# Performance work log

Hardware: AMD Instinct MI355X
Metric: run time of the kernel (lower is better)

The kernel has to match this reference:

```python
import jax, jax.numpy as jnp
import numpy as np

L, B, T, C, H, V, CTX = 4, 2, 1024, 1024, 16, 50257, 2048
D = C // H
EPS = 1e-5
NEG_SLOPE = 0.01


def layer_norm(x, w, b):
    mu = jnp.mean(x, axis=-1, keepdims=True)
    var = jnp.mean(jnp.square(x - mu), axis=-1, keepdims=True)
    return (x - mu) * jax.lax.rsqrt(var + EPS) * w + b


def setup_inputs() -> dict:
    key = jax.random.key(0)
    ks = jax.random.split(key, 8)
    s = 0.02  # init std as in _init_weights
    return {
        "idx": jax.random.randint(ks[0], (B, T), 0, V),
        "wte": jax.random.normal(ks[1], (V, C), jnp.float32) * s,
        "wpe": jax.random.normal(ks[2], (CTX, C), jnp.float32) * s,
        "ln1_w": jnp.ones((L, C), jnp.float32),
        "ln1_b": jnp.zeros((L, C), jnp.float32),
        "attn_w": jax.random.normal(ks[3], (L, C, 3 * C), jnp.float32) * s,
        "attn_b": jnp.zeros((L, 3 * C), jnp.float32),
        "proj_w": jax.random.normal(ks[4], (L, C, C), jnp.float32) * s,
        "proj_b": jnp.zeros((L, C), jnp.float32),
        "ln2_w": jnp.ones((L, C), jnp.float32),
        "ln2_b": jnp.zeros((L, C), jnp.float32),
        "fc_w": jax.random.normal(ks[5], (L, C, 4 * C), jnp.float32) * s,
        "fc_b": jnp.zeros((L, 4 * C), jnp.float32),
        "fcproj_w": jax.random.normal(ks[6], (L, 4 * C, C), jnp.float32) * s,
        "fcproj_b": jnp.zeros((L, C), jnp.float32),
        "lnf_w": jnp.ones((C,), jnp.float32),
        "lnf_b": jnp.zeros((C,), jnp.float32),
    }


def reference(idx, wte, wpe, ln1_w, ln1_b, attn_w, attn_b, proj_w, proj_b,
              ln2_w, ln2_b, fc_w, fc_b, fcproj_w, fcproj_b, lnf_w, lnf_b):
    t = idx.shape[1]
    x = wte[idx] + wpe[:t]  # [B,T,C]; dropout=0 => identity
    causal = jnp.tril(jnp.ones((t, t), bool))  # [T,T]
    scale = 1.0 / np.sqrt(D)
    for l in range(L):
        # --- causal self-attention ---
        h = layer_norm(x, ln1_w[l], ln1_b[l])
        qkv = h @ attn_w[l] + attn_b[l]  # [B,T,3C]
        q, k, v = jnp.split(qkv, 3, axis=-1)
        q = q.reshape(B, t, H, D)
        k = k.reshape(B, t, H, D)
        v = v.reshape(B, t, H, D)
        att = jnp.einsum('bthd,bshd->bhts', q, k) * scale  # [B,H,T,T]
        att = jnp.where(causal, att, -jnp.inf)
        att = jax.nn.softmax(att, axis=-1)
        y = jnp.einsum('bhts,bshd->bthd', att, v).reshape(B, t, C)
        x = x + y @ proj_w[l] + proj_b[l]
        # --- MLP ---
        h = layer_norm(x, ln2_w[l], ln2_b[l])
        h = h @ fc_w[l] + fc_b[l]
        h = jnp.where(h >= 0, h, NEG_SLOPE * h)  # LeakyReLU(0.01)
        x = x + h @ fcproj_w[l] + fcproj_b[l]
    x = layer_norm(x, lnf_w, lnf_b)
    # targets=None path: lm_head on last position only, tied weight = wte
    logits = x[:, -1:, :] @ wte.T  # [B,1,V]
    return logits
```

## Files before the change

kernel.cpp:

```cpp
#include <hip/hip_runtime.h>
#include <hip/hip_bf16.h>


#define TT 1024
#define CC 1024
#define NHEAD 16
#define DHEAD 64
#define NBATCH 2
#define VOCAB 50257

typedef __attribute__((ext_vector_type(8))) short bf16x8;
typedef __attribute__((ext_vector_type(4))) float f32x4;
typedef __attribute__((ext_vector_type(16))) float f32x16;

#define GPTR(p) (const __attribute__((address_space(1))) void*)(p)
#define LPTR(p) (__attribute__((address_space(3))) void*)(p)

__device__ __forceinline__ unsigned short f2bf(float f) {
  union { float f; unsigned u; } v; v.f = f;
  unsigned r = v.u + 0x7fffu + ((v.u >> 16) & 1u);
  return (unsigned short)(r >> 16);
}
__device__ __forceinline__ float bf2f(unsigned short u) {
  union { unsigned u; float f; } v; v.u = ((unsigned)u) << 16;
  return v.f;
}

__device__ __forceinline__ f32x4 mfma_bf16(bf16x8 a, bf16x8 b, f32x4 c) {
  return __builtin_amdgcn_mfma_f32_16x16x32_bf16(a, b, c, 0, 0, 0);
}
__device__ __forceinline__ f32x16 mfma32_bf16(bf16x8 a, bf16x8 b, f32x16 c) {
  return __builtin_amdgcn_mfma_f32_32x32x16_bf16(a, b, c, 0, 0, 0);
}

__device__ __forceinline__ unsigned pk2(float lo, float hi) {
  return (unsigned)f2bf(lo) | ((unsigned)f2bf(hi) << 16);
}

__global__ __launch_bounds__(256) void embedln_k(const int* __restrict__ idx,
    const float* __restrict__ wte, const float* __restrict__ wpe,
    const float* __restrict__ lw, const float* __restrict__ lb,
    float* __restrict__ x, unsigned short* __restrict__ h)
{
  __shared__ float rs[4], rss[4];
  const int row = blockIdx.x;
  const int t = row & (TT - 1);
  const int tok = idx[row];
  const int tid = threadIdx.x, wave = tid >> 6, lane = tid & 63;
  float4 va = ((const float4*)(wte + (size_t)tok * CC))[tid];
  float4 vp = ((const float4*)(wpe + (size_t)t * CC))[tid];
  float4 v = make_float4(va.x + vp.x, va.y + vp.y, va.z + vp.z, va.w + vp.w);
  ((float4*)(x + (size_t)row * CC))[tid] = v;
  float s  = v.x + v.y + v.z + v.w;
  float ss = v.x*v.x + v.y*v.y + v.z*v.z + v.w*v.w;
#pragma unroll
  for (int off = 1; off < 64; off <<= 1) {
    s  += __shfl_xor(s, off, 64);
    ss += __shfl_xor(ss, off, 64);
  }
  if (lane == 0) { rs[wave] = s; rss[wave] = ss; }
  __syncthreads();
  s  = rs[0] + rs[1] + rs[2] + rs[3];
  ss = rss[0] + rss[1] + rss[2] + rss[3];
  float mu = s * (1.f / CC);
  float var = ss * (1.f / CC) - mu * mu;
  float rstd = rsqrtf(var + 1e-5f);
  float4 wv = ((const float4*)lw)[tid];
  float4 bv = ((const float4*)lb)[tid];
  float o0 = (v.x - mu) * rstd * wv.x + bv.x;
  float o1 = (v.y - mu) * rstd * wv.y + bv.y;
  float o2 = (v.z - mu) * rstd * wv.z + bv.z;
  float o3 = (v.w - mu) * rstd * wv.w + bv.w;
  ((uint2*)(h + (size_t)row * CC))[tid] = make_uint2(pk2(o0, o1), pk2(o2, o3));
}

__global__ __launch_bounds__(256) void redln_k(float* __restrict__ x,
    const unsigned short* __restrict__ P, const float* __restrict__ bias,
    const float* __restrict__ lw, const float* __restrict__ lb,
    unsigned short* __restrict__ out, int splits)
{
  int row = blockIdx.x * 4 + (threadIdx.x >> 6);
  int lane = threadIdx.x & 63;
  const int c0 = lane * 16;
  float* xw = x + (size_t)row * CC + c0;
  float4 v[4];
#pragma unroll
  for (int i = 0; i < 4; ++i) v[i] = *(const float4*)(xw + i * 4);
  {
    const float4* b4 = (const float4*)(bias + c0);
#pragma unroll
    for (int i = 0; i < 4; ++i) {
      float4 bv = b4[i];
      v[i].x += bv.x; v[i].y += bv.y; v[i].z += bv.z; v[i].w += bv.w;
    }
  }
  for (int sp = 0; sp < splits; ++sp) {
    const unsigned short* pp = P + ((size_t)sp * 2048 + row) * CC + c0;
    bf16x8 pa = *(const bf16x8*)pp;
    bf16x8 pb = *(const bf16x8*)(pp + 8);
    v[0].x += bf2f((unsigned short)pa[0]); v[0].y += bf2f((unsigned short)pa[1]);
    v[0].z += bf2f((unsigned short)pa[2]); v[0].w += bf2f((unsigned short)pa[3]);
    v[1].x += bf2f((unsigned short)pa[4]); v[1].y += bf2f((unsigned short)pa[5]);
    v[1].z += bf2f((unsigned short)pa[6]); v[1].w += bf2f((unsigned short)pa[7]);
    v[2].x += bf2f((unsigned short)pb[0]); v[2].y += bf2f((unsigned short)pb[1]);
    v[2].z += bf2f((unsigned short)pb[2]); v[2].w += bf2f((unsigned short)pb[3]);
    v[3].x += bf2f((unsigned short)pb[4]); v[3].y += bf2f((unsigned short)pb[5]);
    v[3].z += bf2f((unsigned short)pb[6]); v[3].w += bf2f((unsigned short)pb[7]);
  }
  float s = 0.f, ss = 0.f;
#pragma unroll
  for (int i = 0; i < 4; ++i) {
    *(float4*)(xw + i * 4) = v[i];
    s  += v[i].x + v[i].y + v[i].z + v[i].w;
    ss += v[i].x*v[i].x + v[i].y*v[i].y + v[i].z*v[i].z + v[i].w*v[i].w;
  }
#pragma unroll
  for (int off = 1; off < 64; off <<= 1) {
    s  += __shfl_xor(s, off, 64);
    ss += __shfl_xor(ss, off, 64);
  }
  float mu = s * (1.f / CC);
  float var = ss * (1.f / CC) - mu * mu;
  float rstd = rsqrtf(var + 1e-5f);
  const float* wr = lw + c0;
  const float* br = lb + c0;
  unsigned q[8];
#pragma unroll
  for (int i = 0; i < 4; ++i) {
    float4 wv = *(const float4*)(wr + i * 4);
    float4 bv = *(const float4*)(br + i * 4);
    float o0 = (v[i].x - mu) * rstd * wv.x + bv.x;
    float o1 = (v[i].y - mu) * rstd * wv.y + bv.y;
    float o2 = (v[i].z - mu) * rstd * wv.z + bv.z;
    float o3 = (v[i].w - mu) * rstd * wv.w + bv.w;
    q[i*2+0] = pk2(o0, o1);
    q[i*2+1] = pk2(o2, o3);
  }
  uint4* op = (uint4*)(out + (size_t)row * CC + c0);
  op[0] = make_uint4(q[0], q[1], q[2], q[3]);
  op[1] = make_uint4(q[4], q[5], q[6], q[7]);
}

__global__ __launch_bounds__(256) void wconv_all_k(
    const float* __restrict__ attn_w, unsigned short* __restrict__ wt_attn,
    const float* __restrict__ proj_w, unsigned short* __restrict__ wt_proj,
    const float* __restrict__ fc_w,   unsigned short* __restrict__ wt_fc,
    const float* __restrict__ fcp_w,  unsigned short* __restrict__ wt_fcp)
{
  int b = blockIdx.x;
  const float* W; unsigned short* Wt; int K, N, kx, ny;
  if (b < 3072) {
    int layer = b / 768, tI = b % 768;
    K = 1024; N = 3072;
    W = attn_w + (size_t)layer * K * N; Wt = wt_attn + (size_t)layer * K * N;
    kx = tI % 16; ny = tI / 16;
  } else if (b < 3840) {
    b -= 3072; int layer = b / 256, tI = b % 256;
    K = 1024; N = 1024;
    W = proj_w + (size_t)layer * K * N; Wt = wt_proj + (size_t)layer * K * N;
    kx = tI % 16; ny = tI / 16;
  } else if (b < 6912) {
    b -= 3840; int layer = b / 1024, tI = b % 1024;
    K = 1024; N = 4096;
    W = fc_w + (size_t)layer * K * N; Wt = wt_fc + (size_t)layer * K * N;
    kx = tI % 16; ny = tI / 16;
  } else {
    b -= 6912; int layer = b / 1024, tI = b % 1024;
    K = 4096; N = 1024;
    W = fcp_w + (size_t)layer * K * N; Wt = wt_fcp + (size_t)layer * K * N;
    kx = tI % 64; ny = tI / 64;
  }
  __shared__ float tile[64][65];
  const int k0 = kx << 6, n0 = ny << 6;
  const int t = threadIdx.x;
  {
    const int r = t >> 4, c4 = t & 15;
#pragma unroll
    for (int p = 0; p < 4; ++p) {
      int kr = r + (p << 4);
      float4 v = *(const float4*)(W + (size_t)(k0 + kr) * N + n0 + (c4 << 2));
      tile[kr][(c4 << 2) + 0] = v.x;
      tile[kr][(c4 << 2) + 1] = v.y;
      tile[kr][(c4 << 2) + 2] = v.z;
      tile[kr][(c4 << 2) + 3] = v.w;
    }
  }
  __syncthreads();
  {
    const int n = t >> 2, kq = t & 3;
    bf16x8 o0, o1;
#pragma unroll
    for (int e = 0; e < 8; ++e) o0[e] = (short)f2bf(tile[(kq << 4) + e][n]);
#pragma unroll
    for (int e = 0; e < 8; ++e) o1[e] = (short)f2bf(tile[(kq << 4) + 8 + e][n]);
    unsigned short* dst = Wt + (size_t)(n0 + n) * K + k0 + (kq << 4);
    *(bf16x8*)dst = o0;
    *(bf16x8*)(dst + 8) = o1;
  }
}

#define MODE_QKV  0
#define MODE_PART 1
#define MODE_FC   2

template<int MODE>
__global__ __launch_bounds__(256, 4) void gemm_k(
    const unsigned short* __restrict__ A,
    const unsigned short* __restrict__ Wt,
    const float* __restrict__ bias,
    unsigned short* __restrict__ obf,
    unsigned short* __restrict__ q_o,
    unsigned short* __restrict__ k_o,
    unsigned short* __restrict__ v_o,
    int M, int N, int K, int kchunk, int ncol0)
{
  __shared__ alignas(16) unsigned short Asm[128 * 64];
  __shared__ alignas(16) unsigned short Bsm[128 * 64];
  const int tid  = threadIdx.x;
  const int wave = tid >> 6, lane = tid & 63;
  const int rl = lane & 31, hi = lane >> 5;
  const int nTM = M >> 7, nTN = N >> 7;
  int bid = blockIdx.x;
  const int mt = bid % nTM; bid /= nTM;
  const int nt = bid % nTN;
  const int s  = bid / nTN;
  const int m0 = mt << 7, n0 = nt << 7;
  const int kb = s * kchunk;
  const int nIter = kchunk >> 6;
  const int wm = (wave >> 1) << 6, wn = (wave & 1) << 6;
  f32x16 acc[2][2] = {};

#define STAGE(K0)                                                             \
  {                                                                           \
    _Pragma("unroll")                                                         \
    for (int c = 0; c < 4; ++c) {                                             \
      const int seg = (wave << 2) + c;                                        \
      const int g = (seg << 6) + lane;                                        \
      const int row = g >> 3, kq = g & 7;                                     \
      const int kqs = kq ^ (row & 7);                                         \
      const unsigned short* asrc = A  + (size_t)(m0 + row) * K + (K0) + (kqs << 3); \
      const unsigned short* bsrc = Wt + (size_t)(n0 + row) * K + (K0) + (kqs << 3); \
      __builtin_amdgcn_global_load_lds(GPTR(asrc), LPTR(&Asm[seg << 9]), 16, 0, 0); \
      __builtin_amdgcn_global_load_lds(GPTR(bsrc), LPTR(&Bsm[seg << 9]), 16, 0, 0); \
    }                                                                         \
  }

  for (int t = 0; t < nIter; ++t) {
    STAGE(kb + (t << 6));
    __syncthreads();
#pragma unroll
    for (int sl = 0; sl < 4; ++sl) {
      const int c = sl * 2 + hi;
      const int cs = (c ^ (rl & 7)) << 3;
      bf16x8 a0 = *(const bf16x8*)(Asm + ((wm + rl) << 6) + cs);
      bf16x8 a1 = *(const bf16x8*)(Asm + ((wm + 32 + rl) << 6) + cs);
      bf16x8 b0 = *(const bf16x8*)(Bsm + ((wn + rl) << 6) + cs);
      bf16x8 b1 = *(const bf16x8*)(Bsm + ((wn + 32 + rl) << 6) + cs);
      acc[0][0] = mfma32_bf16(a0, b0, acc[0][0]);
      acc[0][1] = mfma32_bf16(a0, b1, acc[0][1]);
      acc[1][0] = mfma32_bf16(a1, b0, acc[1][0]);
      acc[1][1] = mfma32_bf16(a1, b1, acc[1][1]);
    }
    __syncthreads();
  }
#undef STAGE

#pragma unroll
  for (int j = 0; j < 2; ++j) {
    int gc = n0 + wn + j * 32 + rl;
    int gcol = ncol0 + gc;
    float bv = (MODE == MODE_PART) ? 0.f : bias[gcol];
#pragma unroll
    for (int i = 0; i < 2; ++i) {
      int gr0 = m0 + wm + i * 32 + 4 * hi;
#pragma unroll
      for (int reg = 0; reg < 16; ++reg) {
        int grow = gr0 + (reg & 3) + 8 * (reg >> 2);
        float val = acc[i][j][reg] + bv;
        if (MODE == MODE_QKV) {
          int which = gcol >> 10;
          int head = (gcol >> 6) & 15;
          int d = gcol & 63;
          int bb = grow >> 10, tt2 = grow & (TT - 1);
          size_t bhb = ((size_t)((bb << 4) + head)) << 16;
          if (which == 2)      v_o[bhb + ((size_t)d << 10) + tt2] = f2bf(val);
          else if (which == 1) k_o[bhb + ((size_t)tt2 << 6) + d] = f2bf(val);
          else                 q_o[bhb + ((size_t)tt2 << 6) + d] = f2bf(val);
        } else if (MODE == MODE_FC) {
          val = (val >= 0.f) ? val : 0.01f * val;
          obf[(size_t)grow * N + gc] = f2bf(val);
        } else {
          obf[((size_t)s * M + grow) * N + gc] = f2bf(val);
        }
      }
    }
  }
}

__global__ __launch_bounds__(256) void attn_k(
    const unsigned short* __restrict__ Qb,
    const unsigned short* __restrict__ Kb,
    const unsigned short* __restrict__ Vb,
    unsigned short* __restrict__ ybuf)
{
  __shared__ alignas(16) unsigned short Ksm[64][72];
  __shared__ alignas(16) unsigned short Vtsm[64][64];
  __shared__ alignas(16) unsigned short Psm[4][16][72];
  const int tid = threadIdx.x;
  const int wave = tid >> 6, lane = tid & 63;
  const int lg = lane >> 4, ll = lane & 15;
  const int qt = blockIdx.x & 15, bh = blockIdx.x >> 4;
  const int b = bh >> 4, h = bh & 15;
  const size_t base = (size_t)bh << 16;
  const int q0 = qt << 6;
  const float SC = 0.125f * 1.44269504f;

  const int qrow = q0 + wave * 16 + ll;
  bf16x8 aq0 = *(const bf16x8*)(Qb + base + ((size_t)qrow << 6) + (lg << 3));
  bf16x8 aq1 = *(const bf16x8*)(Qb + base + ((size_t)qrow << 6) + 32 + (lg << 3));

  f32x4 accy[4] = {};
  float m_run[4], l_run[4];
#pragma unroll
  for (int r = 0; r < 4; ++r) { m_run[r] = -1e30f; l_run[r] = 0.f; }

  const int sk_row = tid >> 3, sk_cq = tid & 7;
  const int sv_d = tid & 63, sv_kq = tid >> 6;
  const int qg0 = q0 + wave * 16 + (lg << 2);

  for (int kb = 0; kb <= qt; ++kb) {
    const int kbase = kb << 6;
#pragma unroll
    for (int p = 0; p < 2; ++p) {
      int r = sk_row + (p << 5);
      bf16x8 kv = *(const bf16x8*)(Kb + base + ((size_t)(kbase + r) << 6) + (sk_cq << 3));
      *(bf16x8*)&Ksm[r][sk_cq << 3] = kv;
    }
#pragma unroll
    for (int p = 0; p < 2; ++p) {
      int kq8 = sv_kq + (p << 2);
      bf16x8 wv = *(const bf16x8*)(Vb + base + ((size_t)sv_d << 10) + kbase + (kq8 << 3));
      int u = kq8 ^ (sv_d & 7);
      *(bf16x8*)&Vtsm[sv_d][u << 3] = wv;
    }
    __syncthreads();

    float p_[4][4];
    float rmax[4] = {-1e30f, -1e30f, -1e30f, -1e30f};
    __builtin_amdgcn_s_setprio(1);
#pragma unroll
    for (int kk = 0; kk < 4; ++kk) {
      f32x4 z = {};
      bf16x8 bk0 = *(const bf16x8*)&Ksm[kk * 16 + ll][lg << 3];
      bf16x8 bk1 = *(const bf16x8*)&Ksm[kk * 16 + ll][32 + (lg << 3)];
      z = mfma_bf16(aq0, bk0, z);
      z = mfma_bf16(aq1, bk1, z);
      int key = kbase + kk * 16 + ll;
#pragma unroll
      for (int r = 0; r < 4; ++r) {
        float v = z[r] * SC;
        v = (key > qg0 + r) ? -1e30f : v;
        p_[kk][r] = v;
        rmax[r] = fmaxf(rmax[r], v);
      }
    }
    __builtin_amdgcn_s_setprio(0);
#pragma unroll
    for (int off = 1; off < 16; off <<= 1)
#pragma unroll
      for (int r = 0; r < 4; ++r)
        rmax[r] = fmaxf(rmax[r], __shfl_xor(rmax[r], off, 64));

    float alpha[4], rsum[4];
#pragma unroll
    for (int r = 0; r < 4; ++r) {
      float mn = fmaxf(m_run[r], rmax[r]);
      alpha[r] = exp2f(m_run[r] - mn);
      m_run[r] = mn;
      rsum[r] = 0.f;
    }
#pragma unroll
    for (int kk = 0; kk < 4; ++kk)
#pragma unroll
      for (int r = 0; r < 4; ++r) {
        float e = exp2f(p_[kk][r] - m_run[r]);
        p_[kk][r] = e;
        rsum[r] += e;
      }
#pragma unroll
    for (int off = 1; off < 16; off <<= 1)
#pragma unroll
      for (int r = 0; r < 4; ++r)
        rsum[r] += __shfl_xor(rsum[r], off, 64);
#pragma unroll
    for (int r = 0; r < 4; ++r)
      l_run[r] = l_run[r] * alpha[r] + rsum[r];
#pragma unroll
    for (int df = 0; df < 4; ++df)
#pragma unroll
      for (int r = 0; r < 4; ++r)
        accy[df][r] *= alpha[r];

#pragma unroll
    for (int kk = 0; kk < 4; ++kk)
#pragma unroll
      for (int r = 0; r < 4; ++r)
        Psm[wave][(lg << 2) + r][kk * 16 + ll] = f2bf(p_[kk][r]);
    bf16x8 pa0 = *(const bf16x8*)&Psm[wave][ll][lg << 3];
    bf16x8 pa1 = *(const bf16x8*)&Psm[wave][ll][32 + (lg << 3)];

    __builtin_amdgcn_s_setprio(1);
#pragma unroll
    for (int df = 0; df < 4; ++df) {
      int d = df * 16 + ll;
      int u0 = lg ^ (d & 7);
      int u1 = (4 + lg) ^ (d & 7);
      bf16x8 bv0 = *(const bf16x8*)&Vtsm[d][u0 << 3];
      bf16x8 bv1 = *(const bf16x8*)&Vtsm[d][u1 << 3];
      accy[df] = mfma_bf16(pa0, bv0, accy[df]);
      accy[df] = mfma_bf16(pa1, bv1, accy[df]);
    }
    __builtin_amdgcn_s_setprio(0);
    __syncthreads();
  }

#pragma unroll
  for (int df = 0; df < 4; ++df)
#pragma unroll
    for (int r = 0; r < 4; ++r) {
      int qr = qg0 + r;
      float y = accy[df][r] / l_run[r];
      ybuf[(((size_t)((b << 10) + qr)) << 10) + (h << 6) + df * 16 + ll] = f2bf(y);
    }
}


__global__ __launch_bounds__(256) void qlast_k(
    const unsigned short* __restrict__ hbuf,
    const float* __restrict__ Wq,
    float* __restrict__ qpart)
{
  __shared__ float xs[2][128];
  const int tid = threadIdx.x, ks = blockIdx.y;
  {
    const int b = tid >> 7, j = tid & 127;
    xs[b][j] = bf2f(hbuf[((size_t)(b * TT + TT - 1)) * CC + ks * 128 + j]);
  }
  __syncthreads();
  const int n = blockIdx.x * 256 + tid;
  float a0 = 0.f, a1 = 0.f;
  const float* wp = Wq + (size_t)(ks * 128) * 3072 + n;
  for (int k = 0; k < 128; k += 8)
#pragma unroll
    for (int u = 0; u < 8; ++u) {
      float w = wp[(size_t)(k + u) * 3072];
      a0 += xs[0][k + u] * w;
      a1 += xs[1][k + u] * w;
    }
  qpart[(size_t)(ks * 2 + 0) * 1024 + n] = a0;
  qpart[(size_t)(ks * 2 + 1) * 1024 + n] = a1;
}

__global__ __launch_bounds__(256) void attnlast2_k(
    const float* __restrict__ qpart, const float* __restrict__ bq,
    const unsigned short* __restrict__ Kb,
    const unsigned short* __restrict__ Vb,
    float* __restrict__ y_last)
{
  __shared__ float qs[64];
  __shared__ float wm[4], wl[4], wacc[4][64];
  const int tid = threadIdx.x;
  const int wave = tid >> 6, lane = tid & 63;
  const int bh = blockIdx.x;
  const int b = bh >> 4, h = bh & 15;
  const size_t base = (size_t)bh << 16;
  if (tid < 64) {
    const int col = h * 64 + tid;
    float q = bq[col];
#pragma unroll
    for (int ks = 0; ks < 8; ++ks)
      q += qpart[(size_t)(ks * 2 + b) * 1024 + col];
    qs[tid] = q;
  }
  __syncthreads();

  float m_w = -1e30f, l_w = 0.f, acc = 0.f;
  for (int ks = 0; ks < 4; ++ks) {
    const int key = ks * 256 + wave * 64 + lane;
    float s = 0.f;
    const unsigned short* kp = Kb + base + ((size_t)key << 6);
#pragma unroll
    for (int o = 0; o < 8; ++o) {
      bf16x8 kv = *(const bf16x8*)(kp + (o << 3));
#pragma unroll
      for (int e = 0; e < 8; ++e)
        s += qs[(o << 3) + e] * bf2f((unsigned short)kv[e]);
    }
    s *= 0.125f;
    float m = s;
#pragma unroll
    for (int off = 1; off < 64; off <<= 1)
      m = fmaxf(m, __shfl_xor(m, off, 64));
    float mn = fmaxf(m_w, m);
    float alpha = __expf(m_w - mn);
    m_w = mn;
    float p = __expf(s - mn);
    float ps = p;
#pragma unroll
    for (int off = 1; off < 64; off <<= 1)
      ps += __shfl_xor(ps, off, 64);
    l_w = l_w * alpha + ps;
    float a2 = 0.f;
    const unsigned short* vp = Vb + base + ((size_t)lane << 10) + ks * 256 + wave * 64;
#pragma unroll
    for (int j8 = 0; j8 < 8; ++j8) {
      bf16x8 vv = *(const bf16x8*)(vp + (j8 << 3));
#pragma unroll
      for (int e = 0; e < 8; ++e) {
        float pj = __shfl(p, (j8 << 3) + e, 64);
        a2 += pj * bf2f((unsigned short)vv[e]);
      }
    }
    acc = acc * alpha + a2;
  }
  if (lane == 0) { wm[wave] = m_w; wl[wave] = l_w; }
  wacc[wave][lane] = acc;
  __syncthreads();
  if (wave == 0) {
    float m0 = fmaxf(fmaxf(wm[0], wm[1]), fmaxf(wm[2], wm[3]));
    float lt = 0.f, at = 0.f;
#pragma unroll
    for (int sI = 0; sI < 4; ++sI) {
      float f = __expf(wm[sI] - m0);
      lt += wl[sI] * f;
      at += wacc[sI][lane] * f;
    }
    y_last[b * CC + h * 64 + lane] = at / lt;
  }
}

__global__ __launch_bounds__(256) void projpart_k(
    const float* __restrict__ ylast,
    const float* __restrict__ W,
    float* __restrict__ ppart)
{
  __shared__ float xs[2][128];
  const int tid = threadIdx.x, ks = blockIdx.y;
  {
    const int b = tid >> 7, j = tid & 127;
    xs[b][j] = ylast[b * 1024 + ks * 128 + j];
  }
  __syncthreads();
  const int n = blockIdx.x * 256 + tid;
  float a0 = 0.f, a1 = 0.f;
  const float* wp = W + (size_t)(ks * 128) * 1024 + n;
  for (int k = 0; k < 128; k += 8)
#pragma unroll
    for (int u = 0; u < 8; ++u) {
      float w = wp[(size_t)(k + u) * 1024];
      a0 += xs[0][k + u] * w;
      a1 += xs[1][k + u] * w;
    }
  ppart[(size_t)(ks * 2 + 0) * 1024 + n] = a0;
  ppart[(size_t)(ks * 2 + 1) * 1024 + n] = a1;
}

__global__ __launch_bounds__(256) void fclast_k(
    const float* __restrict__ x, const float* __restrict__ ppart,
    const float* __restrict__ pbias,
    const float* __restrict__ lw, const float* __restrict__ lb,
    const float* __restrict__ W,
    float* __restrict__ fcpart)
{
  __shared__ float xs[2][1024];
  const int tid = threadIdx.x;
  const int wave = tid >> 6, lane = tid & 63;
  if (wave < 2) {
    const int c0 = lane * 16;
    const float* xr = x + ((size_t)(wave * TT + TT - 1)) * CC + c0;
    float4 v[4];
    float s = 0.f, ss = 0.f;
#pragma unroll
    for (int i = 0; i < 4; ++i) {
      v[i] = *(const float4*)(xr + i * 4);
      float4 bv = *(const float4*)(pbias + c0 + i * 4);
      v[i].x += bv.x; v[i].y += bv.y; v[i].z += bv.z; v[i].w += bv.w;
    }
#pragma unroll
    for (int sp = 0; sp < 8; ++sp) {
      const float* pp = ppart + (size_t)(sp * 2 + wave) * 1024 + c0;
#pragma unroll
      for (int i = 0; i < 4; ++i) {
        float4 pv = *(const float4*)(pp + i * 4);
        v[i].x += pv.x; v[i].y += pv.y; v[i].z += pv.z; v[i].w += pv.w;
      }
    }
#pragma unroll
    for (int i = 0; i < 4; ++i) {
      s  += v[i].x + v[i].y + v[i].z + v[i].w;
      ss += v[i].x*v[i].x + v[i].y*v[i].y + v[i].z*v[i].z + v[i].w*v[i].w;
    }
#pragma unroll
    for (int off = 1; off < 64; off <<= 1) {
      s  += __shfl_xor(s, off, 64);
      ss += __shfl_xor(ss, off, 64);
    }
    float mu = s * (1.f / CC);
    float var = ss * (1.f / CC) - mu * mu;
    float rstd = rsqrtf(var + 1e-5f);
#pragma unroll
    for (int i = 0; i < 4; ++i) {
      float4 wv = *(const float4*)(lw + c0 + i * 4);
      float4 bv = *(const float4*)(lb + c0 + i * 4);
      xs[wave][c0 + i * 4 + 0] = (v[i].x - mu) * rstd * wv.x + bv.x;
      xs[wave][c0 + i * 4 + 1] = (v[i].y - mu) * rstd * wv.y + bv.y;
      xs[wave][c0 + i * 4 + 2] = (v[i].z - mu) * rstd * wv.z + bv.z;
      xs[wave][c0 + i * 4 + 3] = (v[i].w - mu) * rstd * wv.w + bv.w;
    }
  }
  __syncthreads();
  const int ks = blockIdx.y;
  const int n = blockIdx.x * 256 + tid;
  float a0 = 0.f, a1 = 0.f;
  const float* wp = W + (size_t)(ks * 128) * 4096 + n;
  for (int k = 0; k < 128; k += 8)
#pragma unroll
    for (int u = 0; u < 8; ++u) {
      float w = wp[(size_t)(k + u) * 4096];
      a0 += xs[0][ks * 128 + k + u] * w;
      a1 += xs[1][ks * 128 + k + u] * w;
    }
  fcpart[(size_t)(ks * 2 + 0) * 4096 + n] = a0;
  fcpart[(size_t)(ks * 2 + 1) * 4096 + n] = a1;
}

__global__ __launch_bounds__(256) void fcprojpart_k(
    const float* __restrict__ fcpart, const float* __restrict__ fcbias,
    const float* __restrict__ W,
    float* __restrict__ fppart)
{
  __shared__ float hs[2][512];
  const int tid = threadIdx.x, ks = blockIdx.y;
#pragma unroll
  for (int i = 0; i < 4; ++i) {
    const int e = tid + 256 * i;
    const int b = e >> 9, j = e & 511;
    const int c = ks * 512 + j;
    float v = fcbias[c];
#pragma unroll
    for (int sp = 0; sp < 8; ++sp)
      v += fcpart[(size_t)(sp * 2 + b) * 4096 + c];
    hs[b][j] = (v >= 0.f) ? v : 0.01f * v;
  }
  __syncthreads();
  const int n = blockIdx.x * 256 + tid;
  float a0 = 0.f, a1 = 0.f;
  const float* wp = W + (size_t)(ks * 512) * 1024 + n;
  for (int k = 0; k < 512; k += 8)
#pragma unroll
    for (int u = 0; u < 8; ++u) {
      float w = wp[(size_t)(k + u) * 1024];
      a0 += hs[0][k + u] * w;
      a1 += hs[1][k + u] * w;
    }
  fppart[(size_t)(ks * 2 + 0) * 1024 + n] = a0;
  fppart[(size_t)(ks * 2 + 1) * 1024 + n] = a1;
}

__global__ __launch_bounds__(256) void lnfmerge_k(const float* __restrict__ x,
    const float* __restrict__ ppart, const float* __restrict__ pbias,
    const float* __restrict__ fppart, const float* __restrict__ fpbias,
    const float* __restrict__ lw, const float* __restrict__ lb,
    float* __restrict__ xf)
{
  __shared__ float rs[4], rss[4];
  const int row = blockIdx.x;
  const int tid = threadIdx.x;
  const int wave = tid >> 6, lane = tid & 63;
  const int c0 = tid * 4;
  float4 v = *(const float4*)(x + ((size_t)(row * TT + TT - 1)) * CC + c0);
  {
    float4 b1 = *(const float4*)(pbias + c0);
    float4 b2 = *(const float4*)(fpbias + c0);
    v.x += b1.x + b2.x; v.y += b1.y + b2.y;
    v.z += b1.z + b2.z; v.w += b1.w + b2.w;
  }
#pragma unroll
  for (int sp = 0; sp < 8; ++sp) {
    float4 a = *(const float4*)(ppart + (size_t)(sp * 2 + row) * 1024 + c0);
    float4 b = *(const float4*)(fppart + (size_t)(sp * 2 + row) * 1024 + c0);
    v.x += a.x + b.x; v.y += a.y + b.y;
    v.z += a.z + b.z; v.w += a.w + b.w;
  }
  float s  = v.x + v.y + v.z + v.w;
  float ss = v.x*v.x + v.y*v.y + v.z*v.z + v.w*v.w;
#pragma unroll
  for (int off = 1; off < 64; off <<= 1) {
    s  += __shfl_xor(s, off, 64);
    ss += __shfl_xor(ss, off, 64);
  }
  if (lane == 0) { rs[wave] = s; rss[wave] = ss; }
  __syncthreads();
  s  = rs[0] + rs[1] + rs[2] + rs[3];
  ss = rss[0] + rss[1] + rss[2] + rss[3];
  float mu = s * (1.f / CC);
  float var = ss * (1.f / CC) - mu * mu;
  float rstd = rsqrtf(var + 1e-5f);
  float4 wv = *(const float4*)(lw + c0);
  float4 bv = *(const float4*)(lb + c0);
  float4 o;
  o.x = (v.x - mu) * rstd * wv.x + bv.x;
  o.y = (v.y - mu) * rstd * wv.y + bv.y;
  o.z = (v.z - mu) * rstd * wv.z + bv.z;
  o.w = (v.w - mu) * rstd * wv.w + bv.w;
  *(float4*)(xf + (size_t)row * CC + c0) = o;
}

__global__ __launch_bounds__(256) void head_k(const float* __restrict__ xf,
    const float* __restrict__ wte, float* __restrict__ out)
{
  int v = (blockIdx.x << 2) + (threadIdx.x >> 6);
  if (v >= VOCAB) return;
  int lane = threadIdx.x & 63;
  const float4* wr = (const float4*)(wte + (size_t)v * CC);
  const float4* x0 = (const float4*)xf;
  const float4* x1 = (const float4*)(xf + CC);
  float a0 = 0.f, a1 = 0.f;
#pragma unroll
  for (int i = 0; i < 4; ++i) {
    float4 wv = wr[lane + i * 64];
    float4 p0 = x0[lane + i * 64];
    float4 p1 = x1[lane + i * 64];
    a0 += wv.x * p0.x + wv.y * p0.y + wv.z * p0.z + wv.w * p0.w;
    a1 += wv.x * p1.x + wv.y * p1.y + wv.z * p1.z + wv.w * p1.w;
  }
#pragma unroll
  for (int off = 1; off < 64; off <<= 1) {
    a0 += __shfl_xor(a0, off, 64);
    a1 += __shfl_xor(a1, off, 64);
  }
  if (lane == 0) {
    out[v] = a0;
    out[VOCAB + v] = a1;
  }
}

extern "C" void kernel_launch(void* const* d_in, const int* in_sizes, int n_in,
                              void* d_out, int out_size, void* d_ws, size_t ws_size,
                              hipStream_t stream)
{
  const int*   idx      = (const int*)d_in[0];
  const float* wte      = (const float*)d_in[1];
  const float* wpe      = (const float*)d_in[2];
  const float* ln1_w    = (const float*)d_in[3];
  const float* ln1_b    = (const float*)d_in[4];
  const float* attn_w   = (const float*)d_in[5];
  const float* attn_b   = (const float*)d_in[6];
  const float* proj_w   = (const float*)d_in[7];
  const float* proj_b   = (const float*)d_in[8];
  const float* ln2_w    = (const float*)d_in[9];
  const float* ln2_b    = (const float*)d_in[10];
  const float* fc_w     = (const float*)d_in[11];
  const float* fc_b     = (const float*)d_in[12];
  const float* fcproj_w = (const float*)d_in[13];
  const float* fcproj_b = (const float*)d_in[14];
  const float* lnf_w    = (const float*)d_in[15];
  const float* lnf_b    = (const float*)d_in[16];
  float* out = (float*)d_out;

  const size_t MB = 1u << 20;
  char* ws = (char*)d_ws;
  float*          x   = (float*)ws;
  unsigned short* h   = (unsigned short*)(ws + 8*MB);
  unsigned short* qb  = (unsigned short*)(ws + 12*MB);
  unsigned short* kb_ = (unsigned short*)(ws + 16*MB);
  unsigned short* vb  = (unsigned short*)(ws + 20*MB);
  unsigned short* yb  = (unsigned short*)(ws + 24*MB);
  unsigned short* hf  = (unsigned short*)(ws + 28*MB);
  char* sm = ws + 44*MB;
  float* xf     = (float*)(sm + 0);
  float* ylast  = (float*)(sm + 16*1024);
  float* qpart  = (float*)(sm + 64*1024);
  float* ppart  = (float*)(sm + 128*1024);
  float* fppart = (float*)(sm + 192*1024);
  float* fcpart = (float*)(sm + 256*1024);
  unsigned short* wt_attn   = (unsigned short*)(ws + 46*MB);
  unsigned short* wt_proj   = (unsigned short*)(ws + 70*MB);
  unsigned short* wt_fc     = (unsigned short*)(ws + 76*MB);
  unsigned short* wt_fcproj = (unsigned short*)(ws + 100*MB);
  unsigned short* Ppart     = (unsigned short*)(ws + 124*MB);

  embedln_k<<<NBATCH * TT, 256, 0, stream>>>(idx, wte, wpe, ln1_w, ln1_b, x, h);

  wconv_all_k<<<9984, 256, 0, stream>>>(attn_w, wt_attn, proj_w, wt_proj,
                                        fc_w, wt_fc, fcproj_w, wt_fcproj);

  for (int l = 0; l < 3; ++l) {
    gemm_k<MODE_QKV><<<16 * 24, 256, 0, stream>>>(h,
        wt_attn + (size_t)l * 3072 * 1024, attn_b + (size_t)l * 3 * CC,
        nullptr, qb, kb_, vb, 2048, 3072, 1024, 1024, 0);
    attn_k<<<NBATCH * NHEAD * 16, 256, 0, stream>>>(qb, kb_, vb, yb);
    gemm_k<MODE_PART><<<16 * 8 * 4, 256, 0, stream>>>(yb,
        wt_proj + (size_t)l * 1024 * 1024, nullptr,
        Ppart, nullptr, nullptr, nullptr, 2048, 1024, 1024, 256, 0);
    redln_k<<<512, 256, 0, stream>>>(x, Ppart, proj_b + l * CC,
        ln2_w + l * CC, ln2_b + l * CC, h, 4);
    gemm_k<MODE_FC><<<16 * 32, 256, 0, stream>>>(h,
        wt_fc + (size_t)l * 1024 * 4096, fc_b + (size_t)l * 4 * CC,
        hf, nullptr, nullptr, nullptr, 2048, 4096, 1024, 1024, 0);
    gemm_k<MODE_PART><<<16 * 8 * 4, 256, 0, stream>>>(hf,
        wt_fcproj + (size_t)l * 4096 * 1024, nullptr,
        Ppart, nullptr, nullptr, nullptr, 2048, 1024, 4096, 1024, 0);
    redln_k<<<512, 256, 0, stream>>>(x, Ppart, fcproj_b + l * CC,
        ln1_w + (l + 1) * CC, ln1_b + (l + 1) * CC, h, 4);
  }

  {
    const int l = 3;
    gemm_k<MODE_QKV><<<16 * 16, 256, 0, stream>>>(h,
        wt_attn + (size_t)l * 3072 * 1024 + (size_t)1024 * 1024,
        attn_b + (size_t)l * 3 * CC,
        nullptr, qb, kb_, vb, 2048, 2048, 1024, 1024, 1024);
    qlast_k<<<dim3(4, 8), 256, 0, stream>>>(h,
        attn_w + (size_t)l * CC * 3 * CC, qpart);
    attnlast2_k<<<32, 256, 0, stream>>>(qpart, attn_b + (size_t)l * 3 * CC,
        kb_, vb, ylast);
    projpart_k<<<dim3(4, 8), 256, 0, stream>>>(ylast,
        proj_w + (size_t)l * CC * CC, ppart);
    fclast_k<<<dim3(16, 8), 256, 0, stream>>>(x, ppart, proj_b + l * CC,
        ln2_w + l * CC, ln2_b + l * CC,
        fc_w + (size_t)l * CC * 4 * CC, fcpart);
    fcprojpart_k<<<dim3(4, 8), 256, 0, stream>>>(fcpart,
        fc_b + (size_t)l * 4 * CC, fcproj_w + (size_t)l * 4 * CC * CC, fppart);
    lnfmerge_k<<<2, 256, 0, stream>>>(x, ppart, proj_b + l * CC,
        fppart, fcproj_b + l * CC, lnf_w, lnf_b, xf);
  }

  head_k<<<(VOCAB + 3) / 4, 256, 0, stream>>>(xf, wte, out);
}
```

Measured before the change: 644.9 us.

## Fuse embed+weight-convert launches; widen attention key tile and skip rescale

```diff
diff --git a/kernel.cpp b/kernel.cpp
--- a/kernel.cpp
+++ b/kernel.cpp
@@ -37,117 +37,50 @@
   return (unsigned)f2bf(lo) | ((unsigned)f2bf(hi) << 16);
 }
 
-__global__ __launch_bounds__(256) void embedln_k(const int* __restrict__ idx,
+__global__ __launch_bounds__(256) void prep_k(const int* __restrict__ idx,
     const float* __restrict__ wte, const float* __restrict__ wpe,
     const float* __restrict__ lw, const float* __restrict__ lb,
-    float* __restrict__ x, unsigned short* __restrict__ h)
-{
-  __shared__ float rs[4], rss[4];
-  const int row = blockIdx.x;
-  const int t = row & (TT - 1);
-  const int tok = idx[row];
-  const int tid = threadIdx.x, wave = tid >> 6, lane = tid & 63;
-  float4 va = ((const float4*)(wte + (size_t)tok * CC))[tid];
-  float4 vp = ((const float4*)(wpe + (size_t)t * CC))[tid];
-  float4 v = make_float4(va.x + vp.x, va.y + vp.y, va.z + vp.z, va.w + vp.w);
-  ((float4*)(x + (size_t)row * CC))[tid] = v;
-  float s  = v.x + v.y + v.z + v.w;
-  float ss = v.x*v.x + v.y*v.y + v.z*v.z + v.w*v.w;
-#pragma unroll
-  for (int off = 1; off < 64; off <<= 1) {
-    s  += __shfl_xor(s, off, 64);
-    ss += __shfl_xor(ss, off, 64);
-  }
-  if (lane == 0) { rs[wave] = s; rss[wave] = ss; }
-  __syncthreads();
-  s  = rs[0] + rs[1] + rs[2] + rs[3];
-  ss = rss[0] + rss[1] + rss[2] + rss[3];
-  float mu = s * (1.f / CC);
-  float var = ss * (1.f / CC) - mu * mu;
-  float rstd = rsqrtf(var + 1e-5f);
-  float4 wv = ((const float4*)lw)[tid];
-  float4 bv = ((const float4*)lb)[tid];
-  float o0 = (v.x - mu) * rstd * wv.x + bv.x;
-  float o1 = (v.y - mu) * rstd * wv.y + bv.y;
-  float o2 = (v.z - mu) * rstd * wv.z + bv.z;
-  float o3 = (v.w - mu) * rstd * wv.w + bv.w;
-  ((uint2*)(h + (size_t)row * CC))[tid] = make_uint2(pk2(o0, o1), pk2(o2, o3));
-}
-
-__global__ __launch_bounds__(256) void redln_k(float* __restrict__ x,
-    const unsigned short* __restrict__ P, const float* __restrict__ bias,
-    const float* __restrict__ lw, const float* __restrict__ lb,
-    unsigned short* __restrict__ out, int splits)
-{
-  int row = blockIdx.x * 4 + (threadIdx.x >> 6);
-  int lane = threadIdx.x & 63;
-  const int c0 = lane * 16;
-  float* xw = x + (size_t)row * CC + c0;
-  float4 v[4];
-#pragma unroll
-  for (int i = 0; i < 4; ++i) v[i] = *(const float4*)(xw + i * 4);
-  {
-    const float4* b4 = (const float4*)(bias + c0);
-#pragma unroll
-    for (int i = 0; i < 4; ++i) {
-      float4 bv = b4[i];
-      v[i].x += bv.x; v[i].y += bv.y; v[i].z += bv.z; v[i].w += bv.w;
-    }
-  }
-  for (int sp = 0; sp < splits; ++sp) {
-    const unsigned short* pp = P + ((size_t)sp * 2048 + row) * CC + c0;
-    bf16x8 pa = *(const bf16x8*)pp;
-    bf16x8 pb = *(const bf16x8*)(pp + 8);
-    v[0].x += bf2f((unsigned short)pa[0]); v[0].y += bf2f((unsigned short)pa[1]);
-    v[0].z += bf2f((unsigned short)pa[2]); v[0].w += bf2f((unsigned short)pa[3]);
-    v[1].x += bf2f((unsigned short)pa[4]); v[1].y += bf2f((unsigned short)pa[5]);
-    v[1].z += bf2f((unsigned short)pa[6]); v[1].w += bf2f((unsigned short)pa[7]);
-    v[2].x += bf2f((unsigned short)pb[0]); v[2].y += bf2f((unsigned short)pb[1]);
-    v[2].z += bf2f((unsigned short)pb[2]); v[2].w += bf2f((unsigned short)pb[3]);
-    v[3].x += bf2f((unsigned short)pb[4]); v[3].y += bf2f((unsigned short)pb[5]);
-    v[3].z += bf2f((unsigned short)pb[6]); v[3].w += bf2f((unsigned short)pb[7]);
-  }
-  float s = 0.f, ss = 0.f;
-#pragma unroll
-  for (int i = 0; i < 4; ++i) {
-    *(float4*)(xw + i * 4) = v[i];
-    s  += v[i].x + v[i].y + v[i].z + v[i].w;
-    ss += v[i].x*v[i].x + v[i].y*v[i].y + v[i].z*v[i].z + v[i].w*v[i].w;
-  }
-#pragma unroll
-  for (int off = 1; off < 64; off <<= 1) {
-    s  += __shfl_xor(s, off, 64);
-    ss += __shfl_xor(ss, off, 64);
-  }
-  float mu = s * (1.f / CC);
-  float var = ss * (1.f / CC) - mu * mu;
-  float rstd = rsqrtf(var + 1e-5f);
-  const float* wr = lw + c0;
-  const float* br = lb + c0;
-  unsigned q[8];
-#pragma unroll
-  for (int i = 0; i < 4; ++i) {
-    float4 wv = *(const float4*)(wr + i * 4);
-    float4 bv = *(const float4*)(br + i * 4);
-    float o0 = (v[i].x - mu) * rstd * wv.x + bv.x;
-    float o1 = (v[i].y - mu) * rstd * wv.y + bv.y;
-    float o2 = (v[i].z - mu) * rstd * wv.z + bv.z;
-    float o3 = (v[i].w - mu) * rstd * wv.w + bv.w;
-    q[i*2+0] = pk2(o0, o1);
-    q[i*2+1] = pk2(o2, o3);
-  }
-  uint4* op = (uint4*)(out + (size_t)row * CC + c0);
-  op[0] = make_uint4(q[0], q[1], q[2], q[3]);
-  op[1] = make_uint4(q[4], q[5], q[6], q[7]);
-}
-
-__global__ __launch_bounds__(256) void wconv_all_k(
+    float* __restrict__ x, unsigned short* __restrict__ h,
     const float* __restrict__ attn_w, unsigned short* __restrict__ wt_attn,
     const float* __restrict__ proj_w, unsigned short* __restrict__ wt_proj,
     const float* __restrict__ fc_w,   unsigned short* __restrict__ wt_fc,
     const float* __restrict__ fcp_w,  unsigned short* __restrict__ wt_fcp)
 {
-  int b = blockIdx.x;
+  __shared__ float tile[64][65];
+  const int tid = threadIdx.x;
+  if (blockIdx.x < 2048) {
+    const int row = blockIdx.x;
+    const int t = row & (TT - 1);
+    const int tok = idx[row];
+    const int wave = tid >> 6, lane = tid & 63;
+    float4 va = ((const float4*)(wte + (size_t)tok * CC))[tid];
+    float4 vp = ((const float4*)(wpe + (size_t)t * CC))[tid];
+    float4 v = make_float4(va.x + vp.x, va.y + vp.y, va.z + vp.z, va.w + vp.w);
+    ((float4*)(x + (size_t)row * CC))[tid] = v;
+    float s  = v.x + v.y + v.z + v.w;
+    float ss = v.x*v.x + v.y*v.y + v.z*v.z + v.w*v.w;
+#pragma unroll
+    for (int off = 1; off < 64; off <<= 1) {
+      s  += __shfl_xor(s, off, 64);
+      ss += __shfl_xor(ss, off, 64);
+    }
+    if (lane == 0) { tile[0][wave] = s; tile[0][4 + wave] = ss; }
+    __syncthreads();
+    s  = tile[0][0] + tile[0][1] + tile[0][2] + tile[0][3];
+    ss = tile[0][4] + tile[0][5] + tile[0][6] + tile[0][7];
+    float mu = s * (1.f / CC);
+    float var = ss * (1.f / CC) - mu * mu;
+    float rstd = rsqrtf(var + 1e-5f);
+    float4 wv = ((const float4*)lw)[tid];
+    float4 bv = ((const float4*)lb)[tid];
+    float o0 = (v.x - mu) * rstd * wv.x + bv.x;
+    float o1 = (v.y - mu) * rstd * wv.y + bv.y;
+    float o2 = (v.z - mu) * rstd * wv.z + bv.z;
+    float o3 = (v.w - mu) * rstd * wv.w + bv.w;
+    ((uint2*)(h + (size_t)row * CC))[tid] = make_uint2(pk2(o0, o1), pk2(o2, o3));
+    return;
+  }
+  int b = blockIdx.x - 2048;
   const float* W; unsigned short* Wt; int K, N, kx, ny;
   if (b < 3072) {
     int layer = b / 768, tI = b % 768;
@@ -170,11 +103,9 @@
     W = fcp_w + (size_t)layer * K * N; Wt = wt_fcp + (size_t)layer * K * N;
     kx = tI % 64; ny = tI / 64;
   }
-  __shared__ float tile[64][65];
   const int k0 = kx << 6, n0 = ny << 6;
-  const int t = threadIdx.x;
   {
-    const int r = t >> 4, c4 = t & 15;
+    const int r = tid >> 4, c4 = tid & 15;
 #pragma unroll
     for (int p = 0; p < 4; ++p) {
       int kr = r + (p << 4);
@@ -187,7 +118,7 @@
   }
   __syncthreads();
   {
-    const int n = t >> 2, kq = t & 3;
+    const int n = tid >> 2, kq = tid & 3;
     bf16x8 o0, o1;
 #pragma unroll
     for (int e = 0; e < 8; ++e) o0[e] = (short)f2bf(tile[(kq << 4) + e][n]);
@@ -197,6 +128,73 @@
     *(bf16x8*)dst = o0;
     *(bf16x8*)(dst + 8) = o1;
   }
+}
+
+__global__ __launch_bounds__(256) void redln_k(float* __restrict__ x,
+    const unsigned short* __restrict__ P, const float* __restrict__ bias,
+    const float* __restrict__ lw, const float* __restrict__ lb,
+    unsigned short* __restrict__ out, int splits)
+{
+  int row = blockIdx.x * 4 + (threadIdx.x >> 6);
+  int lane = threadIdx.x & 63;
+  const int c0 = lane * 16;
+  float* xw = x + (size_t)row * CC + c0;
+  float4 v[4];
+#pragma unroll
+  for (int i = 0; i < 4; ++i) v[i] = *(const float4*)(xw + i * 4);
+  {
+    const float4* b4 = (const float4*)(bias + c0);
+#pragma unroll
+    for (int i = 0; i < 4; ++i) {
+      float4 bv = b4[i];
+      v[i].x += bv.x; v[i].y += bv.y; v[i].z += bv.z; v[i].w += bv.w;
+    }
+  }
+  for (int sp = 0; sp < splits; ++sp) {
+    const unsigned short* pp = P + ((size_t)sp * 2048 + row) * CC + c0;
+    bf16x8 pa = *(const bf16x8*)pp;
+    bf16x8 pb = *(const bf16x8*)(pp + 8);
+    v[0].x += bf2f((unsigned short)pa[0]); v[0].y += bf2f((unsigned short)pa[1]);
+    v[0].z += bf2f((unsigned short)pa[2]); v[0].w += bf2f((unsigned short)pa[3]);
+    v[1].x += bf2f((unsigned short)pa[4]); v[1].y += bf2f((unsigned short)pa[5]);
+    v[1].z += bf2f((unsigned short)pa[6]); v[1].w += bf2f((unsigned short)pa[7]);
+    v[2].x += bf2f((unsigned short)pb[0]); v[2].y += bf2f((unsigned short)pb[1]);
+    v[2].z += bf2f((unsigned short)pb[2]); v[2].w += bf2f((unsigned short)pb[3]);
+    v[3].x += bf2f((unsigned short)pb[4]); v[3].y += bf2f((unsigned short)pb[5]);
+    v[3].z += bf2f((unsigned short)pb[6]); v[3].w += bf2f((unsigned short)pb[7]);
+  }
+  float s = 0.f, ss = 0.f;
+#pragma unroll
+  for (int i = 0; i < 4; ++i) {
+    *(float4*)(xw + i * 4) = v[i];
+    s  += v[i].x + v[i].y + v[i].z + v[i].w;
+    ss += v[i].x*v[i].x + v[i].y*v[i].y + v[i].z*v[i].z + v[i].w*v[i].w;
+  }
+#pragma unroll
+  for (int off = 1; off < 64; off <<= 1) {
+    s  += __shfl_xor(s, off, 64);
+    ss += __shfl_xor(ss, off, 64);
+  }
+  float mu = s * (1.f / CC);
+  float var = ss * (1.f / CC) - mu * mu;
+  float rstd = rsqrtf(var + 1e-5f);
+  const float* wr = lw + c0;
+  const float* br = lb + c0;
+  unsigned q[8];
+#pragma unroll
+  for (int i = 0; i < 4; ++i) {
+    float4 wv = *(const float4*)(wr + i * 4);
+    float4 bv = *(const float4*)(br + i * 4);
+    float o0 = (v[i].x - mu) * rstd * wv.x + bv.x;
+    float o1 = (v[i].y - mu) * rstd * wv.y + bv.y;
+    float o2 = (v[i].z - mu) * rstd * wv.z + bv.z;
+    float o3 = (v[i].w - mu) * rstd * wv.w + bv.w;
+    q[i*2+0] = pk2(o0, o1);
+    q[i*2+1] = pk2(o2, o3);
+  }
+  uint4* op = (uint4*)(out + (size_t)row * CC + c0);
+  op[0] = make_uint4(q[0], q[1], q[2], q[3]);
+  op[1] = make_uint4(q[4], q[5], q[6], q[7]);
 }
 
 #define MODE_QKV  0
@@ -303,9 +301,9 @@
     const unsigned short* __restrict__ Vb,
     unsigned short* __restrict__ ybuf)
 {
-  __shared__ alignas(16) unsigned short Ksm[64][72];
-  __shared__ alignas(16) unsigned short Vtsm[64][64];
-  __shared__ alignas(16) unsigned short Psm[4][16][72];
+  __shared__ alignas(16) unsigned short Ksm[128][72];
+  __shared__ alignas(16) unsigned short Vtsm[64][128];
+  __shared__ alignas(16) unsigned short Psm[4][16][136];
   const int tid = threadIdx.x;
   const int wave = tid >> 6, lane = tid & 63;
   const int lg = lane >> 4, ll = lane & 15;
@@ -325,43 +323,52 @@
   for (int r = 0; r < 4; ++r) { m_run[r] = -1e30f; l_run[r] = 0.f; }
 
   const int sk_row = tid >> 3, sk_cq = tid & 7;
-  const int sv_d = tid & 63, sv_kq = tid >> 6;
+  const int sv_d = tid & 63, sv_kq0 = tid >> 6;
   const int qg0 = q0 + wave * 16 + (lg << 2);
 
-  for (int kb = 0; kb <= qt; ++kb) {
-    const int kbase = kb << 6;
-#pragma unroll
-    for (int p = 0; p < 2; ++p) {
+  for (int kbase = 0; kbase < q0 + 64; kbase += 128) {
+#pragma unroll
+    for (int p = 0; p < 4; ++p) {
       int r = sk_row + (p << 5);
       bf16x8 kv = *(const bf16x8*)(Kb + base + ((size_t)(kbase + r) << 6) + (sk_cq << 3));
       *(bf16x8*)&Ksm[r][sk_cq << 3] = kv;
     }
 #pragma unroll
-    for (int p = 0; p < 2; ++p) {
-      int kq8 = sv_kq + (p << 2);
+    for (int p = 0; p < 4; ++p) {
+      int kq8 = sv_kq0 + (p << 2);
       bf16x8 wv = *(const bf16x8*)(Vb + base + ((size_t)sv_d << 10) + kbase + (kq8 << 3));
       int u = kq8 ^ (sv_d & 7);
       *(bf16x8*)&Vtsm[sv_d][u << 3] = wv;
     }
     __syncthreads();
 
-    float p_[4][4];
+    int kkmax = ((q0 + 63 - kbase) >> 4) + 1;
+    if (kkmax > 8) kkmax = 8;
+    const int kkmax2 = (kkmax + 1) & ~1;
+    const int jmax = kkmax2 >> 1;
+
+    float p_[8][4];
     float rmax[4] = {-1e30f, -1e30f, -1e30f, -1e30f};
     __builtin_amdgcn_s_setprio(1);
 #pragma unroll
-    for (int kk = 0; kk < 4; ++kk) {
-      f32x4 z = {};
-      bf16x8 bk0 = *(const bf16x8*)&Ksm[kk * 16 + ll][lg << 3];
-      bf16x8 bk1 = *(const bf16x8*)&Ksm[kk * 16 + ll][32 + (lg << 3)];
-      z = mfma_bf16(aq0, bk0, z);
-      z = mfma_bf16(aq1, bk1, z);
-      int key = kbase + kk * 16 + ll;
-#pragma unroll
-      for (int r = 0; r < 4; ++r) {
-        float v = z[r] * SC;
-        v = (key > qg0 + r) ? -1e30f : v;
-        p_[kk][r] = v;
-        rmax[r] = fmaxf(rmax[r], v);
+    for (int kk = 0; kk < 8; ++kk) {
+      if (kk < kkmax) {
+        f32x4 z = {};
+        bf16x8 bk0 = *(const bf16x8*)&Ksm[kk * 16 + ll][lg << 3];
+        bf16x8 bk1 = *(const bf16x8*)&Ksm[kk * 16 + ll][32 + (lg << 3)];
+        z = mfma_bf16(aq0, bk0, z);
+        z = mfma_bf16(aq1, bk1, z);
+        int key = kbase + kk * 16 + ll;
+#pragma unroll
+        for (int r = 0; r < 4; ++r) {
+          float v = z[r] * SC;
+          v = (key > qg0 + r) ? -1e30f : v;
+          p_[kk][r] = v;
+          rmax[r] = fmaxf(rmax[r], v);
+        }
+      } else {
+#pragma unroll
+        for (int r = 0; r < 4; ++r) p_[kk][r] = -1e30f;
       }
     }
     __builtin_amdgcn_s_setprio(0);
@@ -371,16 +378,21 @@
       for (int r = 0; r < 4; ++r)
         rmax[r] = fmaxf(rmax[r], __shfl_xor(rmax[r], off, 64));
 
-    float alpha[4], rsum[4];
-#pragma unroll
-    for (int r = 0; r < 4; ++r) {
-      float mn = fmaxf(m_run[r], rmax[r]);
-      alpha[r] = exp2f(m_run[r] - mn);
-      m_run[r] = mn;
-      rsum[r] = 0.f;
-    }
-#pragma unroll
-    for (int kk = 0; kk < 4; ++kk)
+    int ok = (rmax[0] <= m_run[0] + 8.f) & (rmax[1] <= m_run[1] + 8.f) &
+             (rmax[2] <= m_run[2] + 8.f) & (rmax[3] <= m_run[3] + 8.f);
+    const int skip = __all(ok);
+    float alpha[4];
+    if (!skip) {
+#pragma unroll
+      for (int r = 0; r < 4; ++r) {
+        float mn = fmaxf(m_run[r], rmax[r]);
+        alpha[r] = exp2f(m_run[r] - mn);
+        m_run[r] = mn;
+      }
+    }
+    float rsum[4] = {0.f, 0.f, 0.f, 0.f};
+#pragma unroll
+    for (int kk = 0; kk < 8; ++kk)
 #pragma unroll
       for (int r = 0; r < 4; ++r) {
         float e = exp2f(p_[kk][r] - m_run[r]);
@@ -392,33 +404,41 @@
 #pragma unroll
       for (int r = 0; r < 4; ++r)
         rsum[r] += __shfl_xor(rsum[r], off, 64);
-#pragma unroll
-    for (int r = 0; r < 4; ++r)
-      l_run[r] = l_run[r] * alpha[r] + rsum[r];
-#pragma unroll
-    for (int df = 0; df < 4; ++df)
+    if (!skip) {
 #pragma unroll
       for (int r = 0; r < 4; ++r)
-        accy[df][r] *= alpha[r];
-
-#pragma unroll
-    for (int kk = 0; kk < 4; ++kk)
+        l_run[r] = l_run[r] * alpha[r] + rsum[r];
+#pragma unroll
+      for (int df = 0; df < 4; ++df)
+#pragma unroll
+        for (int r = 0; r < 4; ++r)
+          accy[df][r] *= alpha[r];
+    } else {
 #pragma unroll
       for (int r = 0; r < 4; ++r)
-        Psm[wave][(lg << 2) + r][kk * 16 + ll] = f2bf(p_[kk][r]);
-    bf16x8 pa0 = *(const bf16x8*)&Psm[wave][ll][lg << 3];
-    bf16x8 pa1 = *(const bf16x8*)&Psm[wave][ll][32 + (lg << 3)];
+        l_run[r] += rsum[r];
+    }
+
+#pragma unroll
+    for (int kk = 0; kk < 8; ++kk)
+      if (kk < kkmax2)
+#pragma unroll
+        for (int r = 0; r < 4; ++r)
+          Psm[wave][(lg << 2) + r][kk * 16 + ll] = f2bf(p_[kk][r]);
 
     __builtin_amdgcn_s_setprio(1);
 #pragma unroll
-    for (int df = 0; df < 4; ++df) {
-      int d = df * 16 + ll;
-      int u0 = lg ^ (d & 7);
-      int u1 = (4 + lg) ^ (d & 7);
-      bf16x8 bv0 = *(const bf16x8*)&Vtsm[d][u0 << 3];
-      bf16x8 bv1 = *(const bf16x8*)&Vtsm[d][u1 << 3];
-      accy[df] = mfma_bf16(pa0, bv0, accy[df]);
-      accy[df] = mfma_bf16(pa1, bv1, accy[df]);
+    for (int j = 0; j < 4; ++j) {
+      if (j < jmax) {
+        bf16x8 pa = *(const bf16x8*)&Psm[wave][ll][j * 32 + (lg << 3)];
+#pragma unroll
+        for (int df = 0; df < 4; ++df) {
+          int d = df * 16 + ll;
+          int u = ((j << 2) + lg) ^ (d & 7);
+          bf16x8 bv = *(const bf16x8*)&Vtsm[d][u << 3];
+          accy[df] = mfma_bf16(pa, bv, accy[df]);
+        }
+      }
     }
     __builtin_amdgcn_s_setprio(0);
     __syncthreads();
@@ -790,10 +810,8 @@
   unsigned short* wt_fcproj = (unsigned short*)(ws + 100*MB);
   unsigned short* Ppart     = (unsigned short*)(ws + 124*MB);
 
-  embedln_k<<<NBATCH * TT, 256, 0, stream>>>(idx, wte, wpe, ln1_w, ln1_b, x, h);
-
-  wconv_all_k<<<9984, 256, 0, stream>>>(attn_w, wt_attn, proj_w, wt_proj,
-                                        fc_w, wt_fc, fcproj_w, wt_fcproj);
+  prep_k<<<2048 + 9984, 256, 0, stream>>>(idx, wte, wpe, ln1_w, ln1_b, x, h,
+      attn_w, wt_attn, proj_w, wt_proj, fc_w, wt_fc, fcproj_w, wt_fcproj);
 
   for (int l = 0; l < 3; ++l) {
     gemm_k<MODE_QKV><<<16 * 24, 256, 0, stream>>>(h,
```

New measurement: 638.5 us. Within noise of the previous version (-1.0%).
